# Kernel optimization log

Measured on AMD Instinct MI355X. Metric: run time of the kernel, lower is better.

Reference implementation:

```python
import jax, jax.numpy as jnp
from jax import lax
import numpy as np

DN = ('NCHW', 'OIHW', 'NCHW')

def _conv(x, w, b):
    y = lax.conv_general_dilated(x, w, (1, 1), 'VALID', dimension_numbers=DN)
    return y + b[None, :, None, None]

def _prelu(x, a):
    return jnp.where(x >= 0, x, a[None, :, None, None] * x)

def _maxpool2(x):
    # MaxPool2d(2,2,ceil_mode=True); spatial dims chosen even so VALID matches.
    return lax.reduce_window(x, -jnp.inf, lax.max, (1, 1, 2, 2), (1, 1, 2, 2), 'VALID')

def setup_inputs() -> dict:
    key = jax.random.key(0)
    ks = jax.random.split(key, 16)
    f = jnp.float32
    x = jax.random.uniform(ks[0], (16, 3, 720, 720), dtype=f) * 255.0
    def w(k, shape, fan_in):
        return jax.random.normal(k, shape, dtype=f) * (1.0 / np.sqrt(fan_in))
    return {
        'x': x,
        'conv1_w': w(ks[1], (10, 3, 3, 3), 27), 'conv1_b': jnp.zeros((10,), f),
        'prelu1_a': jnp.full((10,), 0.25, f),
        'conv2_w': w(ks[2], (16, 10, 3, 3), 90), 'conv2_b': jnp.zeros((16,), f),
        'prelu2_a': jnp.full((16,), 0.25, f),
        'conv3_w': w(ks[3], (32, 16, 3, 3), 144), 'conv3_b': jnp.zeros((32,), f),
        'prelu3_a': jnp.full((32,), 0.25, f),
        'conv41_w': w(ks[4], (2, 32, 1, 1), 32), 'conv41_b': jnp.zeros((2,), f),
        'conv42_w': w(ks[5], (4, 32, 1, 1), 32), 'conv42_b': jnp.zeros((4,), f),
    }

def reference(x, conv1_w, conv1_b, prelu1_a, conv2_w, conv2_b, prelu2_a,
              conv3_w, conv3_b, prelu3_a, conv41_w, conv41_b, conv42_w, conv42_b):
    # MTCNN pixel normalization from detect_p_net
    h = (x - 127.5) * 0.0078125
    h = _prelu(_conv(h, conv1_w, conv1_b), prelu1_a)   # [B,10,718,718]
    h = _maxpool2(h)                                   # [B,10,359,359]
    h = _prelu(_conv(h, conv2_w, conv2_b), prelu2_a)   # [B,16,357,357]
    h = _prelu(_conv(h, conv3_w, conv3_b), prelu3_a)   # [B,32,355,355]
    prob = jax.nn.softmax(_conv(h, conv41_w, conv41_b), axis=1)  # [B,2,355,355]
    reg = _conv(h, conv42_w, conv42_b)                            # [B,4,355,355]
    return (reg, prob)
```

## Files before the change

kernel.cpp:

```cpp
#include <hip/hip_runtime.h>
#include <hip/hip_bf16.h>
#include <cstddef>


#define H1 718
#define PH 359
#define H2 357
#define H3 355

#define W1R_OFF 0
#define B1R_OFF 288
#define AW2_OFF 320
#define BW3_OFF 1600
#define P16_OFF 4096
#define C2H_OFF 16500864

typedef short bf16x8 __attribute__((ext_vector_type(8)));
typedef float f32x4  __attribute__((ext_vector_type(4)));
typedef float f32x16 __attribute__((ext_vector_type(16)));
typedef unsigned short ushort4v __attribute__((ext_vector_type(4)));

__global__ void repack_kernel(const float* __restrict__ w1, const float* __restrict__ b1,
                              const float* __restrict__ w2, const float* __restrict__ w3,
                              float* __restrict__ ws) {
    int t = threadIdx.x;
    const float S = 0.0078125f;
    for (int i = t; i < 270; i += blockDim.x) ws[W1R_OFF + i] = w1[i] * S;
    if (t < 10) {
        float s = 0.f;
        for (int i = 0; i < 27; i++) s += w1[t * 27 + i];
        ws[B1R_OFF + t] = b1[t] - 127.5f * S * s;
    }
    unsigned short* aw2 = (unsigned short*)(ws + AW2_OFF);
    for (int e = t; e < 2560; e += blockDim.x) {
        int s = e >> 9;
        int rem = e & 511;
        int l = rem >> 3, j = rem & 7;
        int q = l >> 4, co = l & 15;
        int tap = 2 * s + (q >> 1);
        int ci  = ((q & 1) << 3) + j;
        float v = (tap < 9 && ci < 10) ? w2[co * 90 + ci * 9 + tap] : 0.f;
        __hip_bfloat16 h = __float2bfloat16(v);
        aw2[e] = *(unsigned short*)&h;
    }
    unsigned short* bw3 = (unsigned short*)(ws + BW3_OFF);
    for (int e = t; e < 4608; e += blockDim.x) {
        int tap = e >> 9;
        int rem = e & 511;
        int l = rem >> 3, j = rem & 7;
        int kh = tap / 3, kw = tap % 3;
        int co = l & 31, ci = ((l >> 5) << 3) + j;
        float v = w3[co * 144 + ci * 9 + kh * 3 + kw];
        __hip_bfloat16 h = __float2bfloat16(v);
        bw3[e] = *(unsigned short*)&h;
    }
}

__global__ void conv1_pool_kernel(const float* __restrict__ x,
                                  const float* __restrict__ ws,
                                  const float* __restrict__ a1,
                                  __hip_bfloat16* __restrict__ p16) {
    int pw = blockIdx.x * blockDim.x + threadIdx.x;
    int ph = blockIdx.y;
    int n  = blockIdx.z;
    if (pw >= PH) return;
    int iy = 2 * ph, ix = 2 * pw;

    float acc[10][4];
    #pragma unroll
    for (int c = 0; c < 10; c++)
        #pragma unroll
        for (int p = 0; p < 4; p++) acc[c][p] = 0.f;

    #pragma unroll
    for (int ci = 0; ci < 3; ci++) {
        const float* xp = x + (((size_t)(n * 3 + ci) * 720 + iy) * 720 + ix);
        float win[4][4];
        #pragma unroll
        for (int r = 0; r < 4; r++) {
            float2 v0 = *(const float2*)(xp + r * 720);
            float2 v1 = *(const float2*)(xp + r * 720 + 2);
            win[r][0] = v0.x; win[r][1] = v0.y; win[r][2] = v1.x; win[r][3] = v1.y;
        }
        #pragma unroll
        for (int c = 0; c < 10; c++) {
            const float* wk = ws + W1R_OFF + c * 27 + ci * 9;
            #pragma unroll
            for (int kh = 0; kh < 3; kh++)
                #pragma unroll
                for (int kw = 0; kw < 3; kw++) {
                    float wv = wk[kh * 3 + kw];
                    acc[c][0] = fmaf(win[kh    ][kw    ], wv, acc[c][0]);
                    acc[c][1] = fmaf(win[kh    ][kw + 1], wv, acc[c][1]);
                    acc[c][2] = fmaf(win[kh + 1][kw    ], wv, acc[c][2]);
                    acc[c][3] = fmaf(win[kh + 1][kw + 1], wv, acc[c][3]);
                }
        }
    }

    __hip_bfloat16 o[16];
    #pragma unroll
    for (int c = 0; c < 10; c++) {
        float b = ws[B1R_OFF + c], al = a1[c];
        float s0 = acc[c][0] + b, s1 = acc[c][1] + b;
        float s2 = acc[c][2] + b, s3 = acc[c][3] + b;
        s0 = s0 >= 0.f ? s0 : al * s0;
        s1 = s1 >= 0.f ? s1 : al * s1;
        s2 = s2 >= 0.f ? s2 : al * s2;
        s3 = s3 >= 0.f ? s3 : al * s3;
        o[c] = __float2bfloat16(fmaxf(fmaxf(s0, s1), fmaxf(s2, s3)));
    }
    #pragma unroll
    for (int c = 10; c < 16; c++) o[c] = __float2bfloat16(0.f);

    float4* dst = (float4*)(p16 + (((size_t)n * PH + ph) * PH + pw) * 16);
    dst[0] = ((float4*)o)[0];
    dst[1] = ((float4*)o)[1];
}

__global__ __launch_bounds__(256)
void conv2_mfma_kernel(const __hip_bfloat16* __restrict__ p16,
                       const float* __restrict__ ws,
                       const float* __restrict__ b2,
                       const float* __restrict__ a2,
                       __hip_bfloat16* __restrict__ c2h) {
    int wv = threadIdx.x >> 6;
    int l  = threadIdx.x & 63;
    int oh  = blockIdx.y * 4 + wv;
    int ow0 = blockIdx.x * 64;
    int n   = blockIdx.z;
    if (oh >= H2) return;

    int pxl = l & 15;
    int q   = l >> 4;
    int taph = q >> 1;
    int choff = (q & 1) << 3;

    const bf16x8* aw = (const bf16x8*)(ws + AW2_OFF);
    bf16x8 afr[5];
    #pragma unroll
    for (int s = 0; s < 5; s++) afr[s] = aw[s * 64 + l];

    bf16x8 zf;
    #pragma unroll
    for (int j = 0; j < 8; j++) zf[j] = 0;

    f32x4 acc[4];
    #pragma unroll
    for (int t = 0; t < 4; t++)
        #pragma unroll
        for (int i = 0; i < 4; i++) acc[t][i] = 0.f;

    #pragma unroll
    for (int s = 0; s < 5; s++) {
        int tap = 2 * s + taph;
        bool real = (tap < 9);
        int kh = tap / 3, kw = tap - kh * 3;
        int ih = oh + kh; if (ih > PH - 1) ih = PH - 1;
        #pragma unroll
        for (int t = 0; t < 4; t++) {
            int iw = ow0 + t * 16 + pxl + kw; if (iw > PH - 1) iw = PH - 1;
            const bf16x8* bp = (const bf16x8*)(p16 + (((size_t)n * PH + ih) * PH + iw) * 16 + choff);
            bf16x8 b = real ? *bp : zf;
            acc[t] = __builtin_amdgcn_mfma_f32_16x16x32_bf16(afr[s], b, acc[t], 0, 0, 0);
        }
    }

    float bb[4], aa[4];
    #pragma unroll
    for (int r = 0; r < 4; r++) { bb[r] = b2[q * 4 + r]; aa[r] = a2[q * 4 + r]; }

    #pragma unroll
    for (int t = 0; t < 4; t++) {
        int px = ow0 + t * 16 + pxl;
        if (px < H2) {
            ushort4v pk;
            #pragma unroll
            for (int r = 0; r < 4; r++) {
                float v = acc[t][r] + bb[r];
                v = v >= 0.f ? v : aa[r] * v;
                __hip_bfloat16 h = __float2bfloat16(v);
                pk[r] = *(unsigned short*)&h;
            }
            *(ushort4v*)(c2h + (((size_t)n * H2 + oh) * H2 + px) * 16 + q * 4) = pk;
        }
    }
}

__global__ __launch_bounds__(256, 1)
void conv3_heads_kernel(const __hip_bfloat16* __restrict__ c2h,
                        const float* __restrict__ ws,
                        const float* __restrict__ b3,
                        const float* __restrict__ a3,
                        const float* __restrict__ w41,
                        const float* __restrict__ b41,
                        const float* __restrict__ w42,
                        const float* __restrict__ b42,
                        float* __restrict__ out) {
    int wv = threadIdx.x >> 6;
    int l  = threadIdx.x & 63;
    int ow0 = blockIdx.x * 32;
    int oh0 = blockIdx.y * 8 + wv * 2;
    int n   = blockIdx.z;

    int m    = l & 31;
    int half = l >> 5;
    int choff = half << 3;

    const bf16x8* bw = (const bf16x8*)(ws + BW3_OFF);
    bf16x8 bfr[9];
    #pragma unroll
    for (int t = 0; t < 9; t++) bfr[t] = bw[t * 64 + l];

    f32x16 acc0, acc1;
    #pragma unroll
    for (int i = 0; i < 16; i++) { acc0[i] = 0.f; acc1[i] = 0.f; }

    #pragma unroll
    for (int kh = 0; kh < 3; kh++) {
        int ih0 = oh0 + kh;     if (ih0 > H2 - 1) ih0 = H2 - 1;
        int ih1 = oh0 + 1 + kh; if (ih1 > H2 - 1) ih1 = H2 - 1;
        #pragma unroll
        for (int kw = 0; kw < 3; kw++) {
            int iw = ow0 + m + kw; if (iw > H2 - 1) iw = H2 - 1;
            const bf16x8* a0p = (const bf16x8*)(c2h + ((((size_t)n * H2 + ih0) * H2 + iw) << 4) + choff);
            const bf16x8* a1p = (const bf16x8*)(c2h + ((((size_t)n * H2 + ih1) * H2 + iw) << 4) + choff);
            bf16x8 a0 = *a0p;
            bf16x8 a1 = *a1p;
            int tap = kh * 3 + kw;
            acc0 = __builtin_amdgcn_mfma_f32_32x32x16_bf16(a0, bfr[tap], acc0, 0, 0, 0);
            acc1 = __builtin_amdgcn_mfma_f32_32x32x16_bf16(a1, bfr[tap], acc1, 0, 0, 0);
        }
    }

    __shared__ float hbuf[4][64 * 33];
    float* hb = hbuf[wv];
    float bb = b3[m], aa = a3[m];
    #pragma unroll
    for (int t = 0; t < 2; t++) {
        #pragma unroll
        for (int r = 0; r < 16; r++) {
            int mprime = (r & 3) + ((r >> 2) << 3) + (half << 2);
            float v = (t ? acc1[r] : acc0[r]) + bb;
            v = v >= 0.f ? v : aa * v;
            hb[(t * 32 + mprime) * 33 + m] = v;
        }
    }
    __syncthreads();

    int poh = oh0 + (l >> 5);
    int pow_ = ow0 + (l & 31);
    float h[32];
    #pragma unroll
    for (int c = 0; c < 32; c++) h[c] = hb[l * 33 + c];

    float l0 = b41[0], l1 = b41[1];
    float r0 = b42[0], r1 = b42[1], r2 = b42[2], r3 = b42[3];
    #pragma unroll
    for (int c = 0; c < 32; c++) {
        float hv = h[c];
        l0 = fmaf(hv, w41[c],      l0);
        l1 = fmaf(hv, w41[32 + c], l1);
        r0 = fmaf(hv, w42[c],      r0);
        r1 = fmaf(hv, w42[32 + c], r1);
        r2 = fmaf(hv, w42[64 + c], r2);
        r3 = fmaf(hv, w42[96 + c], r3);
    }
    float mx  = fmaxf(l0, l1);
    float e0 = __expf(l0 - mx), e1 = __expf(l1 - mx);
    float inv = 1.0f / (e0 + e1);

    if (poh < H3 && pow_ < H3) {
        const size_t sp = (size_t)H3 * H3;
        size_t pos = (size_t)poh * H3 + pow_;
        float* reg  = out;
        float* prob = out + (size_t)16 * 4 * sp;
        reg[((size_t)(n * 4 + 0)) * sp + pos] = r0;
        reg[((size_t)(n * 4 + 1)) * sp + pos] = r1;
        reg[((size_t)(n * 4 + 2)) * sp + pos] = r2;
        reg[((size_t)(n * 4 + 3)) * sp + pos] = r3;
        prob[((size_t)(n * 2 + 0)) * sp + pos] = e0 * inv;
        prob[((size_t)(n * 2 + 1)) * sp + pos] = e1 * inv;
    }
}

extern "C" void kernel_launch(void* const* d_in, const int* in_sizes, int n_in,
                              void* d_out, int out_size, void* d_ws, size_t ws_size,
                              hipStream_t stream) {
    const float* x   = (const float*)d_in[0];
    const float* w1  = (const float*)d_in[1];
    const float* b1  = (const float*)d_in[2];
    const float* a1  = (const float*)d_in[3];
    const float* w2  = (const float*)d_in[4];
    const float* b2  = (const float*)d_in[5];
    const float* a2  = (const float*)d_in[6];
    const float* w3  = (const float*)d_in[7];
    const float* b3  = (const float*)d_in[8];
    const float* a3  = (const float*)d_in[9];
    const float* w41 = (const float*)d_in[10];
    const float* b41 = (const float*)d_in[11];
    const float* w42 = (const float*)d_in[12];
    const float* b42 = (const float*)d_in[13];
    float* out = (float*)d_out;
    float* ws  = (float*)d_ws;

    __hip_bfloat16* p16 = (__hip_bfloat16*)(ws + P16_OFF);
    __hip_bfloat16* c2h = (__hip_bfloat16*)(ws + C2H_OFF);

    repack_kernel<<<1, 256, 0, stream>>>(w1, b1, w2, w3, ws);

    {
        dim3 grid((PH + 127) / 128, PH, 16);
        conv1_pool_kernel<<<grid, 128, 0, stream>>>(x, ws, a1, p16);
    }
    {
        dim3 grid((H2 + 63) / 64, (H2 + 3) / 4, 16);
        conv2_mfma_kernel<<<grid, 256, 0, stream>>>(p16, ws, b2, a2, c2h);
    }
    {
        dim3 grid((H3 + 31) / 32, (H3 + 7) / 8, 16);
        conv3_heads_kernel<<<grid, 256, 0, stream>>>(c2h, ws, b3, a3,
                                                     w41, b41, w42, b42, out);
    }
}
```

Baseline: 313.5 us.

## Stage conv1 input tile in LDS and reduce PReLU+pool via min/max

Conv1+pool now uses a 2D tile of 64x4 pooled outputs per 256-thread block. The block cooperatively loads the 3-channel 10x132 input strip into shared memory with float4 loads, and the convolution reads its windows from LDS instead of overlapping global float2 loads. The bias is folded into the accumulator initialisation. PReLU before max-pool is applied only to the max and min of the four values, since PReLU is monotone for a non-negative slope, which saves per-element selects. The changes add a barrier and LDS use, and the min/max shortcut assumes the slope is non-negative.

```diff
diff --git a/kernel.cpp b/kernel.cpp
--- a/kernel.cpp
+++ b/kernel.cpp
@@ -56,30 +56,63 @@
     }
 }
 
-__global__ void conv1_pool_kernel(const float* __restrict__ x,
-                                  const float* __restrict__ ws,
-                                  const float* __restrict__ a1,
-                                  __hip_bfloat16* __restrict__ p16) {
-    int pw = blockIdx.x * blockDim.x + threadIdx.x;
-    int ph = blockIdx.y;
-    int n  = blockIdx.z;
-    if (pw >= PH) return;
-    int iy = 2 * ph, ix = 2 * pw;
+__global__ __launch_bounds__(256)
+void conv1_pool_kernel(const float* __restrict__ x,
+                       const float* __restrict__ ws,
+                       const float* __restrict__ a1,
+                       __hip_bfloat16* __restrict__ p16) {
+    __shared__ float xs[3][10][132];
+
+    int tid = threadIdx.x;
+    int px0 = blockIdx.x * 64;
+    int py0 = blockIdx.y * 4;
+    int n   = blockIdx.z;
+    int ix0 = 2 * px0;
+    int iy0 = 2 * py0;
+
+    for (int i = tid; i < 990; i += 256) {
+        int r  = i / 33;
+        int c4 = i - r * 33;
+        int ci = r / 10, rr = r - (r / 10) * 10;
+        int gy = iy0 + rr; if (gy > 719) gy = 719;
+        int gx = ix0 + 4 * c4;
+        const float* src = x + (((size_t)(n * 3 + ci) * 720 + gy) * 720);
+        float4 v;
+        if (gx + 3 <= 719) {
+            v = *(const float4*)(src + gx);
+        } else {
+            float q = src[719];
+            v.x = q; v.y = q; v.z = q; v.w = q;
+        }
+        *(float4*)&xs[ci][rr][4 * c4] = v;
+    }
+    __syncthreads();
+
+    int tx = tid & 63;
+    int ty = tid >> 6;
+    int px = px0 + tx;
+    int py = py0 + ty;
+    if (px >= PH || py >= PH) return;
+
+    int lx = 2 * tx;
+    int ly = 2 * ty;
 
     float acc[10][4];
     #pragma unroll
-    for (int c = 0; c < 10; c++)
-        #pragma unroll
-        for (int p = 0; p < 4; p++) acc[c][p] = 0.f;
+    for (int c = 0; c < 10; c++) {
+        float b = ws[B1R_OFF + c];
+        #pragma unroll
+        for (int p = 0; p < 4; p++) acc[c][p] = b;
+    }
 
     #pragma unroll
     for (int ci = 0; ci < 3; ci++) {
-        const float* xp = x + (((size_t)(n * 3 + ci) * 720 + iy) * 720 + ix);
         float win[4][4];
         #pragma unroll
         for (int r = 0; r < 4; r++) {
-            float2 v0 = *(const float2*)(xp + r * 720);
-            float2 v1 = *(const float2*)(xp + r * 720 + 2);
+            const float2* rp = (const float2*)&xs[ci][ly + r][lx];
+            float2 v0 = rp[0];
+            float2 v1 = rp[1];
             win[r][0] = v0.x; win[r][1] = v0.y; win[r][2] = v1.x; win[r][3] = v1.y;
         }
         #pragma unroll
@@ -101,19 +134,17 @@
     __hip_bfloat16 o[16];
     #pragma unroll
     for (int c = 0; c < 10; c++) {
-        float b = ws[B1R_OFF + c], al = a1[c];
-        float s0 = acc[c][0] + b, s1 = acc[c][1] + b;
-        float s2 = acc[c][2] + b, s3 = acc[c][3] + b;
-        s0 = s0 >= 0.f ? s0 : al * s0;
-        s1 = s1 >= 0.f ? s1 : al * s1;
-        s2 = s2 >= 0.f ? s2 : al * s2;
-        s3 = s3 >= 0.f ? s3 : al * s3;
-        o[c] = __float2bfloat16(fmaxf(fmaxf(s0, s1), fmaxf(s2, s3)));
+        float al = a1[c];
+        float mx = fmaxf(fmaxf(acc[c][0], acc[c][1]), fmaxf(acc[c][2], acc[c][3]));
+        float mn = fminf(fminf(acc[c][0], acc[c][1]), fminf(acc[c][2], acc[c][3]));
+        float pa = mx >= 0.f ? mx : al * mx;
+        float pb = mn >= 0.f ? mn : al * mn;
+        o[c] = __float2bfloat16(fmaxf(pa, pb));
     }
     #pragma unroll
     for (int c = 10; c < 16; c++) o[c] = __float2bfloat16(0.f);
 
-    float4* dst = (float4*)(p16 + (((size_t)n * PH + ph) * PH + pw) * 16);
+    float4* dst = (float4*)(p16 + (((size_t)n * PH + py) * PH + px) * 16);
     dst[0] = ((float4*)o)[0];
     dst[1] = ((float4*)o)[1];
 }
@@ -310,8 +341,8 @@
     repack_kernel<<<1, 256, 0, stream>>>(w1, b1, w2, w3, ws);
 
     {
-        dim3 grid((PH + 127) / 128, PH, 16);
-        conv1_pool_kernel<<<grid, 128, 0, stream>>>(x, ws, a1, p16);
+        dim3 grid((PH + 63) / 64, (PH + 3) / 4, 16);
+        conv1_pool_kernel<<<grid, 256, 0, stream>>>(x, ws, a1, p16);
     }
     {
         dim3 grid((H2 + 63) / 64, (H2 + 3) / 4, 16);
```

After: 343.9 us. 1.1x slower.
